# Optimization experiments

Measured on AMD Instinct MI355X. Metric: run time of the kernel, lower is better.

The kernel has to match this reference:

```python
import jax, jax.numpy as jnp
import numpy as np

E = 1024
H = 16
HD = E // H  # 64


def setup_inputs() -> dict:
    key = jax.random.key(0)
    ks = jax.random.split(key, 5)
    x = jax.random.normal(ks[0], (2, 2048, E), dtype=jnp.float32)
    s = 1.0 / np.sqrt(E)
    W_qkv = jax.random.uniform(ks[1], (E, 3 * E), jnp.float32, -s, s)
    b_qkv = jax.random.uniform(ks[2], (3 * E,), jnp.float32, -s, s)
    W_out = jax.random.uniform(ks[3], (E, E), jnp.float32, -s, s)
    b_out = jax.random.uniform(ks[4], (E,), jnp.float32, -s, s)
    return {"x": x, "W_qkv": W_qkv, "b_qkv": b_qkv, "W_out": W_out, "b_out": b_out}


def reference(x, W_qkv, b_qkv, W_out, b_out):
    B, N, _ = x.shape
    scale = HD ** (-0.5)
    qkv = x @ W_qkv + b_qkv                         # [B, N, 3E]
    qkv = qkv.reshape(B, N, H, 3 * HD)              # torch layout: per-head 3*hd chunk
    qkv = qkv.transpose(0, 2, 1, 3)                 # [B, H, N, 3*hd]
    q, k, v = jnp.split(qkv, 3, axis=-1)            # each [B, H, N, hd]
    attn = jnp.einsum('bhqd,bhkd->bhqk', q, k) * scale
    attn = jax.nn.softmax(attn, axis=-1)            # dropout is identity in eval
    out = jnp.einsum('bhqk,bhkd->bhqd', attn, v)    # [B, H, N, hd]
    out = out.transpose(0, 2, 1, 3).reshape(B, N, E)
    return out @ W_out + b_out
```

## Files before the change

kernel.cpp:

```cpp
#include <hip/hip_runtime.h>


#define SEQ 2048
#define NH  16

typedef __attribute__((ext_vector_type(8))) short short8;
typedef __attribute__((ext_vector_type(4))) short short4v;
typedef __attribute__((ext_vector_type(4))) float floatx4;
typedef __attribute__((ext_vector_type(4))) _Float16 half4;
typedef __attribute__((ext_vector_type(2))) _Float16 half2v;
typedef __attribute__((ext_vector_type(2))) __fp16 fp16x2;

#define QSCALE 0.1803368801111204f

__device__ __forceinline__ short f2bf(float f) {
    union { float f; unsigned u; } v; v.f = f;
    unsigned r = v.u + 0x7fffu + ((v.u >> 16) & 1u);
    return (short)(r >> 16);
}

__device__ __forceinline__ float fast_exp2(float x) {
#if __has_builtin(__builtin_amdgcn_exp2f)
    return __builtin_amdgcn_exp2f(x);
#else
    return exp2f(x);
#endif
}

__device__ __forceinline__ half2v cvt_pk(float a, float b) {
#if __has_builtin(__builtin_amdgcn_cvt_pkrtz)
    union { fp16x2 i; half2v o; } u;
    u.i = __builtin_amdgcn_cvt_pkrtz(a, b);
    return u.o;
#else
    half2v r; r.x = (_Float16)a; r.y = (_Float16)b; return r;
#endif
}

#define GLDS16(gp, lp)                                                          \
    __builtin_amdgcn_global_load_lds(                                           \
        (const __attribute__((address_space(1))) unsigned int*)(gp),            \
        (__attribute__((address_space(3))) unsigned int*)(lp), 16, 0, 0)

__global__ __launch_bounds__(256) void cast_f32_bf16_kernel(
    const float* __restrict__ in, short* __restrict__ out)
{
    int i = blockIdx.x * 256 + threadIdx.x;
    const float4* in4 = (const float4*)in + (size_t)i * 2;
    float4 a = in4[0], b = in4[1];
    short8 o = { f2bf(a.x), f2bf(a.y), f2bf(a.z), f2bf(a.w),
                 f2bf(b.x), f2bf(b.y), f2bf(b.z), f2bf(b.w) };
    *((short8*)out + i) = o;
}

__global__ __launch_bounds__(256) void transpose_cast_kernel(
    const float* __restrict__ in, short* __restrict__ out, int R, int C)
{
    __shared__ float T[64][65];
    const int tid = threadIdx.x;
    const int c0 = blockIdx.x * 64, r0 = blockIdx.y * 64;
#pragma unroll
    for (int it = 0; it < 4; ++it) {
        int r = it * 16 + (tid >> 4), c = (tid & 15) * 4;
        float4 v = *(const float4*)(in + (size_t)(r0 + r) * C + c0 + c);
        T[c+0][r] = v.x; T[c+1][r] = v.y; T[c+2][r] = v.z; T[c+3][r] = v.w;
    }
    __syncthreads();
#pragma unroll
    for (int it = 0; it < 4; ++it) {
        int oc = it * 16 + (tid >> 4), k = (tid & 15) * 4;
        short4v o = { f2bf(T[oc][k]), f2bf(T[oc][k+1]), f2bf(T[oc][k+2]), f2bf(T[oc][k+3]) };
        *(short4v*)(out + (size_t)(c0 + oc) * R + r0 + k) = o;
    }
}

__global__ __launch_bounds__(256) void vtrans_kernel(
    const _Float16* __restrict__ vn, _Float16* __restrict__ vt)
{
    __shared__ _Float16 T[64][72];
    const int tid = threadIdx.x;
    const int bh = blockIdx.y, n0 = blockIdx.x * 64;
#pragma unroll
    for (int it = 0; it < 2; ++it) {
        int n = it * 32 + (tid >> 3), c = (tid & 7) * 8;
        const _Float16* p = vn + ((size_t)bh * SEQ + n0 + n) * 64 + c;
        half4 a = *(const half4*)(p);
        half4 b = *(const half4*)(p + 4);
        T[c+0][n] = a.x; T[c+1][n] = a.y; T[c+2][n] = a.z; T[c+3][n] = a.w;
        T[c+4][n] = b.x; T[c+5][n] = b.y; T[c+6][n] = b.z; T[c+7][n] = b.w;
    }
    __syncthreads();
#pragma unroll
    for (int it = 0; it < 2; ++it) {
        int idx = it * 256 + tid;
        int quad = idx & 3, d = (idx >> 2) & 63, u = idx >> 8;
        const _Float16* row = &T[d][u * 32 + quad * 4];
        half4 lo = *(const half4*)(row);
        half4 hi = *(const half4*)(row + 16);
        _Float16* q = vt + ((size_t)bh * 64 + d) * SEQ + n0 + u * 32 + quad * 8;
        *(half4*)(q)     = lo;
        *(half4*)(q + 4) = hi;
    }
}

#define GEMM_CORE(A_PTR, B_PTR, LDA, LDB)                                        \
    __shared__ short As[128 * 32];                                               \
    __shared__ short Bs[128 * 32];                                               \
    const int tid  = threadIdx.x;                                                \
    const int lane = tid & 63, w = tid >> 6;                                     \
    const int quad = lane >> 4, l16 = lane & 15;                                 \
    const int wm = w >> 1, wn = w & 1;                                           \
    const int c0 = blockIdx.x * 128, r0 = blockIdx.y * 128;                      \
    floatx4 acc[4][4];                                                           \
    _Pragma("unroll")                                                            \
    for (int i = 0; i < 4; ++i)                                                  \
        _Pragma("unroll")                                                        \
        for (int j = 0; j < 4; ++j) acc[i][j] = (floatx4){0.f, 0.f, 0.f, 0.f};   \
    const int srow = tid >> 2;                                                   \
    const int sgx  = ((tid & 3) ^ ((srow >> 1) & 3)) * 8;                        \
    const short* Ag = (A_PTR) + (size_t)(r0 + srow) * (LDA) + sgx;               \
    const short* Bg = (B_PTR) + (size_t)(c0 + srow) * (LDB) + sgx;               \
    const int fsw = (l16 >> 1) & 3;                                              \
    for (int kk = 0; kk < 1024; kk += 32) {                                      \
        __syncthreads();                                                         \
        GLDS16(Ag + kk,                      As + tid * 8);                      \
        GLDS16(Ag + (size_t)64 * (LDA) + kk, As + 2048 + tid * 8);               \
        GLDS16(Bg + kk,                      Bs + tid * 8);                      \
        GLDS16(Bg + (size_t)64 * (LDB) + kk, Bs + 2048 + tid * 8);               \
        __syncthreads();                                                         \
        short8 af[4], bf[4];                                                     \
        _Pragma("unroll")                                                        \
        for (int mt = 0; mt < 4; ++mt)                                           \
            af[mt] = *(const short8*)&As[(wm * 64 + mt * 16 + l16) * 32 + (quad ^ fsw) * 8]; \
        _Pragma("unroll")                                                        \
        for (int nt = 0; nt < 4; ++nt)                                           \
            bf[nt] = *(const short8*)&Bs[(wn * 64 + nt * 16 + l16) * 32 + (quad ^ fsw) * 8]; \
        _Pragma("unroll")                                                        \
        for (int mt = 0; mt < 4; ++mt)                                           \
            _Pragma("unroll")                                                    \
            for (int nt = 0; nt < 4; ++nt)                                       \
                acc[mt][nt] = __builtin_amdgcn_mfma_f32_16x16x32_bf16(           \
                    af[mt], bf[nt], acc[mt][nt], 0, 0, 0);                       \
    }

__global__ __launch_bounds__(256) void qkv_gemm_kernel(
    const short* __restrict__ wt, const short* __restrict__ xb,
    const float* __restrict__ bias,
    short* __restrict__ qb, short* __restrict__ kb, _Float16* __restrict__ vnb)
{
    GEMM_CORE(wt, xb, 1024, 1024)
#pragma unroll
    for (int mt = 0; mt < 4; ++mt) {
        int oc0 = r0 + wm * 64 + mt * 16 + quad * 4;
        int head = oc0 / 192;
        int t = (oc0 - head * 192) >> 6;
        int d0 = oc0 & 63;
        float4 bv = *(const float4*)(bias + oc0);
#pragma unroll
        for (int nt = 0; nt < 4; ++nt) {
            int tok = c0 + wn * 64 + nt * 16 + l16;
            int bh = (tok >> 11) * NH + head;
            size_t base = ((size_t)bh * SEQ + (tok & (SEQ - 1))) * 64 + d0;
            float v0 = acc[mt][nt][0] + bv.x, v1 = acc[mt][nt][1] + bv.y;
            float v2 = acc[mt][nt][2] + bv.z, v3 = acc[mt][nt][3] + bv.w;
            if (t == 0) {
                short4v o = { f2bf(v0 * QSCALE), f2bf(v1 * QSCALE),
                              f2bf(v2 * QSCALE), f2bf(v3 * QSCALE) };
                *(short4v*)(qb + base) = o;
            } else if (t == 1) {
                short4v o = { f2bf(v0), f2bf(v1), f2bf(v2), f2bf(v3) };
                *(short4v*)(kb + base) = o;
            } else {
                half4 o = { (_Float16)v0, (_Float16)v1, (_Float16)v2, (_Float16)v3 };
                *(half4*)(vnb + base) = o;
            }
        }
    }
}

__global__ __launch_bounds__(512) void out_gemm_kernel(
    const short* __restrict__ wt, const short* __restrict__ ab,
    const float* __restrict__ bias, float* __restrict__ out)
{
    __shared__ short As[128 * 32];
    __shared__ short Bs[128 * 32];
    const int tid  = threadIdx.x;
    const int lane = tid & 63, w = tid >> 6;
    const int quad = lane >> 4, l16 = lane & 15;
    const int wm = w >> 2, wn = w & 3;
    const int c0 = blockIdx.x * 128, r0 = blockIdx.y * 128;
    floatx4 acc[4][2];
#pragma unroll
    for (int i = 0; i < 4; ++i)
#pragma unroll
        for (int j = 0; j < 2; ++j) acc[i][j] = (floatx4){0.f, 0.f, 0.f, 0.f};
    const int srow = tid >> 2;
    const int sgx  = ((tid & 3) ^ ((srow >> 1) & 3)) * 8;
    const short* Ag = wt + (size_t)(r0 + srow) * 1024 + sgx;
    const short* Bg = ab + (size_t)(c0 + srow) * 1024 + sgx;
    const int fsw = (l16 >> 1) & 3;
    for (int kk = 0; kk < 1024; kk += 32) {
        __syncthreads();
        GLDS16(Ag + kk, As + tid * 8);
        GLDS16(Bg + kk, Bs + tid * 8);
        __syncthreads();
        short8 af[4], bf[2];
#pragma unroll
        for (int mt = 0; mt < 4; ++mt)
            af[mt] = *(const short8*)&As[(wm * 64 + mt * 16 + l16) * 32 + (quad ^ fsw) * 8];
#pragma unroll
        for (int nt = 0; nt < 2; ++nt)
            bf[nt] = *(const short8*)&Bs[(wn * 32 + nt * 16 + l16) * 32 + (quad ^ fsw) * 8];
#pragma unroll
        for (int mt = 0; mt < 4; ++mt)
#pragma unroll
            for (int nt = 0; nt < 2; ++nt)
                acc[mt][nt] = __builtin_amdgcn_mfma_f32_16x16x32_bf16(
                    af[mt], bf[nt], acc[mt][nt], 0, 0, 0);
    }
#pragma unroll
    for (int mt = 0; mt < 4; ++mt) {
        int oc0 = r0 + wm * 64 + mt * 16 + quad * 4;
        float4 bv = *(const float4*)(bias + oc0);
#pragma unroll
        for (int nt = 0; nt < 2; ++nt) {
            int tok = c0 + wn * 32 + nt * 16 + l16;
            float4 o = { acc[mt][nt][0] + bv.x, acc[mt][nt][1] + bv.y,
                         acc[mt][nt][2] + bv.z, acc[mt][nt][3] + bv.w };
            *(float4*)(out + (size_t)tok * 1024 + oc0) = o;
        }
    }
}

__global__ __launch_bounds__(512) void attn_kernel(
    const short* __restrict__ qb, const short* __restrict__ kb,
    const _Float16* __restrict__ vtb, short* __restrict__ ob)
{
    __shared__ short    Ks[128 * 64];
    __shared__ _Float16 Vts[64 * 128];
    __shared__ float    Ls[8][32];
    const int tid  = threadIdx.x;
    const int lane = tid & 63, w = tid >> 6;
    const int quad = lane >> 4, l16 = lane & 15;
    const int qh = w >> 2, kq = w & 3;
    const int bh = blockIdx.x;
    const int q0 = blockIdx.y * 64;

    short8 aq[2][2];
#pragma unroll
    for (int qf = 0; qf < 2; ++qf) {
        const short* qp = qb + ((size_t)bh * SEQ + q0 + qh * 32 + qf * 16 + l16) * 64 + quad * 8;
        aq[qf][0] = *(const short8*)(qp);
        aq[qf][1] = *(const short8*)(qp + 32);
    }

    const int krow = tid >> 3, kg = tid & 7;
    const short* kgp = kb + ((size_t)bh * SEQ + krow) * 64 + (kg ^ (krow & 7)) * 8;
    const int vd = (tid >> 2) & 63, vgg = tid & 3, vu = tid >> 8;
    const _Float16* vgp = vtb + ((size_t)bh * 64 + vd) * SEQ + vu * 32
                        + (vgg ^ ((vd >> 1) & 3)) * 8;

    floatx4 o_acc[4][2];
#pragma unroll
    for (int dt = 0; dt < 4; ++dt)
#pragma unroll
        for (int qf = 0; qf < 2; ++qf) o_acc[dt][qf] = (floatx4){0.f, 0.f, 0.f, 0.f};
    float lw[2] = {0.f, 0.f};

    for (int k0 = 0; k0 < SEQ; k0 += 128) {
        __syncthreads();
        const short* kc_p = kgp + (size_t)k0 * 64;
        GLDS16(kc_p,        Ks + tid * 8);
        GLDS16(kc_p + 4096, Ks + 4096 + tid * 8);
        const _Float16* vc_p = vgp + k0;
        GLDS16((const short*)(vc_p),      (short*)Vts + tid * 8);
        GLDS16((const short*)(vc_p + 64), (short*)Vts + 4096 + tid * 8);
        __syncthreads();

        half4 avlo[4], avhi[4];
#pragma unroll
        for (int dt = 0; dt < 4; ++dt) {
            union { short8 s; struct { half4 lo; half4 hi; } h; } u;
            u.s = *(const short8*)((const short*)Vts + kq * 2048
                    + (dt * 16 + l16) * 32 + (quad ^ ((l16 >> 1) & 3)) * 8);
            avlo[dt] = u.h.lo; avhi[dt] = u.h.hi;
        }

#pragma unroll
        for (int kt = 0; kt < 2; ++kt) {
            const short* krp = &Ks[(kq * 32 + kt * 16 + l16) * 64];
            short8 ak0 = *(const short8*)(krp + ((0 + quad) ^ (l16 & 7)) * 8);
            short8 ak1 = *(const short8*)(krp + ((4 + quad) ^ (l16 & 7)) * 8);
            floatx4 sacc[2];
#pragma unroll
            for (int qf = 0; qf < 2; ++qf) {
                floatx4 z = (floatx4){0.f, 0.f, 0.f, 0.f};
                z = __builtin_amdgcn_mfma_f32_16x16x32_bf16(ak0, aq[qf][0], z, 0, 0, 0);
                sacc[qf] = __builtin_amdgcn_mfma_f32_16x16x32_bf16(ak1, aq[qf][1], z, 0, 0, 0);
            }
            half4 pf[2];
#pragma unroll
            for (int qf = 0; qf < 2; ++qf) {
                float p0 = fast_exp2(sacc[qf][0]);
                float p1 = fast_exp2(sacc[qf][1]);
                float p2 = fast_exp2(sacc[qf][2]);
                float p3 = fast_exp2(sacc[qf][3]);
                lw[qf] += (p0 + p1) + (p2 + p3);
                half2v lo = cvt_pk(p0, p1), hi = cvt_pk(p2, p3);
                pf[qf] = (half4){lo.x, lo.y, hi.x, hi.y};
            }
#pragma unroll
            for (int dt = 0; dt < 4; ++dt)
#pragma unroll
                for (int qf = 0; qf < 2; ++qf)
                    o_acc[dt][qf] = __builtin_amdgcn_mfma_f32_16x16x16f16(
                        kt ? avhi[dt] : avlo[dt], pf[qf], o_acc[dt][qf], 0, 0, 0);
        }
    }

#pragma unroll
    for (int qf = 0; qf < 2; ++qf) {
        lw[qf] += __shfl_xor(lw[qf], 16);
        lw[qf] += __shfl_xor(lw[qf], 32);
        if (quad == 0) Ls[w][qf * 16 + l16] = lw[qf];
    }

    float* RedA = (float*)Ks;
    float* RedB = (float*)Vts;
    __syncthreads();
#pragma unroll
    for (int dt = 0; dt < 4; ++dt)
#pragma unroll
        for (int qf = 0; qf < 2; ++qf) {
            int fi = (((qh * 2 + qf) * 4 + dt) * 64 + lane) * 4;
            if (kq == 2) *(floatx4*)&RedA[fi] = o_acc[dt][qf];
            if (kq == 3) *(floatx4*)&RedB[fi] = o_acc[dt][qf];
        }
    __syncthreads();
    if (kq == 0 || kq == 1) {
#pragma unroll
        for (int dt = 0; dt < 4; ++dt)
#pragma unroll
            for (int qf = 0; qf < 2; ++qf) {
                int fi = (((qh * 2 + qf) * 4 + dt) * 64 + lane) * 4;
                o_acc[dt][qf] += *(const floatx4*)((kq == 0) ? &RedA[fi] : &RedB[fi]);
                if (kq == 1) *(floatx4*)&RedB[fi] = o_acc[dt][qf];
            }
    }
    __syncthreads();
    if (kq == 0) {
        float inv[2];
#pragma unroll
        for (int qf = 0; qf < 2; ++qf) {
            int qi = qf * 16 + l16;
            inv[qf] = 1.0f / (Ls[qh * 4 + 0][qi] + Ls[qh * 4 + 1][qi]
                            + Ls[qh * 4 + 2][qi] + Ls[qh * 4 + 3][qi]);
        }
        const int b = bh >> 4, h = bh & 15;
#pragma unroll
        for (int dt = 0; dt < 4; ++dt)
#pragma unroll
            for (int qf = 0; qf < 2; ++qf) {
                int fi = (((qh * 2 + qf) * 4 + dt) * 64 + lane) * 4;
                floatx4 o = o_acc[dt][qf] + *(const floatx4*)&RedB[fi];
                int tok = b * SEQ + q0 + qh * 32 + qf * 16 + l16;
                short4v o4 = { f2bf(o[0] * inv[qf]), f2bf(o[1] * inv[qf]),
                               f2bf(o[2] * inv[qf]), f2bf(o[3] * inv[qf]) };
                *(short4v*)(ob + (size_t)tok * 1024 + h * 64 + dt * 16 + quad * 4) = o4;
            }
    }
}

extern "C" void kernel_launch(void* const* d_in, const int* in_sizes, int n_in,
                              void* d_out, int out_size, void* d_ws, size_t ws_size,
                              hipStream_t stream) {
    const float* x     = (const float*)d_in[0];
    const float* W_qkv = (const float*)d_in[1];
    const float* b_qkv = (const float*)d_in[2];
    const float* W_out = (const float*)d_in[3];
    const float* b_out = (const float*)d_in[4];
    float* out = (float*)d_out;

    short* xb      = (short*)d_ws;
    short* wqkvt   = xb    + (size_t)4096 * 1024;
    short* woutt   = wqkvt + (size_t)3072 * 1024;
    short* qb      = woutt + (size_t)1024 * 1024;
    short* kb      = qb    + (size_t)32 * SEQ * 64;
    _Float16* vnb  = (_Float16*)(kb + (size_t)32 * SEQ * 64);
    _Float16* vtb  = vnb + (size_t)32 * SEQ * 64;
    short* ob      = (short*)(vtb + (size_t)32 * 64 * SEQ);

    cast_f32_bf16_kernel<<<2048, 256, 0, stream>>>(x, xb);
    transpose_cast_kernel<<<dim3(48, 16), 256, 0, stream>>>(W_qkv, wqkvt, 1024, 3072);
    transpose_cast_kernel<<<dim3(16, 16), 256, 0, stream>>>(W_out, woutt, 1024, 1024);
    qkv_gemm_kernel<<<dim3(32, 24), 256, 0, stream>>>(wqkvt, xb, b_qkv, qb, kb, vnb);
    vtrans_kernel<<<dim3(32, 32), 256, 0, stream>>>(vnb, vtb);
    attn_kernel<<<dim3(32, 32), 512, 0, stream>>>(qb, kb, vtb, ob);
    out_gemm_kernel<<<dim3(32, 8), 512, 0, stream>>>(woutt, ob, b_out, out);
}
```

Measured before the change: 207.0 us.

## Fuse prep kernels and halve attention block size with two KV splits

Merges the x cast and the two weight transpose-casts into one launch dispatched by block index, removing two kernel launches. The attention kernel drops from 512 to 256 threads (4 waves), so each wave handles two 32-key chunks instead of one. The cross-wave reduction shrinks to a single exchange, and a min-blocks hint of 4 is added for occupancy. The grid axes are swapped so q-tiles of the same head are adjacent, which may help K/V cache reuse. Each thread now issues twice as many LDS copies per tile, and the reduction tail is shorter.

```diff
diff --git a/kernel.cpp b/kernel.cpp
--- a/kernel.cpp
+++ b/kernel.cpp
@@ -42,23 +42,31 @@
         (const __attribute__((address_space(1))) unsigned int*)(gp),            \
         (__attribute__((address_space(3))) unsigned int*)(lp), 16, 0, 0)
 
-__global__ __launch_bounds__(256) void cast_f32_bf16_kernel(
-    const float* __restrict__ in, short* __restrict__ out)
-{
-    int i = blockIdx.x * 256 + threadIdx.x;
-    const float4* in4 = (const float4*)in + (size_t)i * 2;
-    float4 a = in4[0], b = in4[1];
-    short8 o = { f2bf(a.x), f2bf(a.y), f2bf(a.z), f2bf(a.w),
-                 f2bf(b.x), f2bf(b.y), f2bf(b.z), f2bf(b.w) };
-    *((short8*)out + i) = o;
-}
-
-__global__ __launch_bounds__(256) void transpose_cast_kernel(
-    const float* __restrict__ in, short* __restrict__ out, int R, int C)
-{
+__global__ __launch_bounds__(256) void prep_kernel(
+    const float* __restrict__ x,  short* __restrict__ xb,
+    const float* __restrict__ wq, short* __restrict__ wqkvt,
+    const float* __restrict__ wo, short* __restrict__ woutt)
+{
+    const int tid = threadIdx.x;
+    const int b = blockIdx.x;
+    if (b < 2048) {
+        int i = b * 256 + tid;
+        const float4* in4 = (const float4*)x + (size_t)i * 2;
+        float4 a = in4[0], c = in4[1];
+        short8 o = { f2bf(a.x), f2bf(a.y), f2bf(a.z), f2bf(a.w),
+                     f2bf(c.x), f2bf(c.y), f2bf(c.z), f2bf(c.w) };
+        *((short8*)xb + i) = o;
+        return;
+    }
     __shared__ float T[64][65];
-    const int tid = threadIdx.x;
-    const int c0 = blockIdx.x * 64, r0 = blockIdx.y * 64;
+    const float* in; short* out; int R, C, c0, r0;
+    if (b < 2816) {
+        int t = b - 2048; in = wq; out = wqkvt; R = 1024; C = 3072;
+        c0 = (t % 48) * 64; r0 = (t / 48) * 64;
+    } else {
+        int t = b - 2816; in = wo; out = woutt; R = 1024; C = 1024;
+        c0 = (t & 15) * 64; r0 = (t >> 4) * 64;
+    }
 #pragma unroll
     for (int it = 0; it < 4; ++it) {
         int r = it * 16 + (tid >> 4), c = (tid & 15) * 4;
@@ -232,19 +240,19 @@
     }
 }
 
-__global__ __launch_bounds__(512) void attn_kernel(
+__global__ __launch_bounds__(256, 4) void attn_kernel(
     const short* __restrict__ qb, const short* __restrict__ kb,
     const _Float16* __restrict__ vtb, short* __restrict__ ob)
 {
     __shared__ short    Ks[128 * 64];
     __shared__ _Float16 Vts[64 * 128];
-    __shared__ float    Ls[8][32];
+    __shared__ float    Ls[4][32];
     const int tid  = threadIdx.x;
     const int lane = tid & 63, w = tid >> 6;
     const int quad = lane >> 4, l16 = lane & 15;
-    const int qh = w >> 2, kq = w & 3;
-    const int bh = blockIdx.x;
-    const int q0 = blockIdx.y * 64;
+    const int qh = w >> 1, kq = w & 1;
+    const int bh = blockIdx.y;
+    const int q0 = blockIdx.x * 64;
 
     short8 aq[2][2];
 #pragma unroll
@@ -256,9 +264,8 @@
 
     const int krow = tid >> 3, kg = tid & 7;
     const short* kgp = kb + ((size_t)bh * SEQ + krow) * 64 + (kg ^ (krow & 7)) * 8;
-    const int vd = (tid >> 2) & 63, vgg = tid & 3, vu = tid >> 8;
-    const _Float16* vgp = vtb + ((size_t)bh * 64 + vd) * SEQ + vu * 32
-                        + (vgg ^ ((vd >> 1) & 3)) * 8;
+    const int vd = tid >> 2, vgg = tid & 3;
+    const _Float16* vgp = vtb + ((size_t)bh * 64 + vd) * SEQ + (vgg ^ ((vd >> 1) & 3)) * 8;
 
     floatx4 o_acc[4][2];
 #pragma unroll
@@ -271,50 +278,57 @@
         __syncthreads();
         const short* kc_p = kgp + (size_t)k0 * 64;
         GLDS16(kc_p,        Ks + tid * 8);
+        GLDS16(kc_p + 2048, Ks + 2048 + tid * 8);
         GLDS16(kc_p + 4096, Ks + 4096 + tid * 8);
+        GLDS16(kc_p + 6144, Ks + 6144 + tid * 8);
         const _Float16* vc_p = vgp + k0;
         GLDS16((const short*)(vc_p),      (short*)Vts + tid * 8);
+        GLDS16((const short*)(vc_p + 32), (short*)Vts + 2048 + tid * 8);
         GLDS16((const short*)(vc_p + 64), (short*)Vts + 4096 + tid * 8);
+        GLDS16((const short*)(vc_p + 96), (short*)Vts + 6144 + tid * 8);
         __syncthreads();
 
-        half4 avlo[4], avhi[4];
-#pragma unroll
-        for (int dt = 0; dt < 4; ++dt) {
-            union { short8 s; struct { half4 lo; half4 hi; } h; } u;
-            u.s = *(const short8*)((const short*)Vts + kq * 2048
-                    + (dt * 16 + l16) * 32 + (quad ^ ((l16 >> 1) & 3)) * 8);
-            avlo[dt] = u.h.lo; avhi[dt] = u.h.hi;
-        }
-
-#pragma unroll
-        for (int kt = 0; kt < 2; ++kt) {
-            const short* krp = &Ks[(kq * 32 + kt * 16 + l16) * 64];
-            short8 ak0 = *(const short8*)(krp + ((0 + quad) ^ (l16 & 7)) * 8);
-            short8 ak1 = *(const short8*)(krp + ((4 + quad) ^ (l16 & 7)) * 8);
-            floatx4 sacc[2];
-#pragma unroll
-            for (int qf = 0; qf < 2; ++qf) {
-                floatx4 z = (floatx4){0.f, 0.f, 0.f, 0.f};
-                z = __builtin_amdgcn_mfma_f32_16x16x32_bf16(ak0, aq[qf][0], z, 0, 0, 0);
-                sacc[qf] = __builtin_amdgcn_mfma_f32_16x16x32_bf16(ak1, aq[qf][1], z, 0, 0, 0);
+#pragma unroll
+        for (int uu = 0; uu < 2; ++uu) {
+            const int u = kq * 2 + uu;
+            half4 avlo[4], avhi[4];
+#pragma unroll
+            for (int dt = 0; dt < 4; ++dt) {
+                union { short8 s; struct { half4 lo; half4 hi; } h; } vv;
+                vv.s = *(const short8*)((const short*)Vts + u * 2048
+                        + (dt * 16 + l16) * 32 + (quad ^ ((l16 >> 1) & 3)) * 8);
+                avlo[dt] = vv.h.lo; avhi[dt] = vv.h.hi;
             }
-            half4 pf[2];
-#pragma unroll
-            for (int qf = 0; qf < 2; ++qf) {
-                float p0 = fast_exp2(sacc[qf][0]);
-                float p1 = fast_exp2(sacc[qf][1]);
-                float p2 = fast_exp2(sacc[qf][2]);
-                float p3 = fast_exp2(sacc[qf][3]);
-                lw[qf] += (p0 + p1) + (p2 + p3);
-                half2v lo = cvt_pk(p0, p1), hi = cvt_pk(p2, p3);
-                pf[qf] = (half4){lo.x, lo.y, hi.x, hi.y};
+#pragma unroll
+            for (int h = 0; h < 2; ++h) {
+                const short* krp = &Ks[(u * 32 + h * 16 + l16) * 64];
+                short8 ak0 = *(const short8*)(krp + ((0 + quad) ^ (l16 & 7)) * 8);
+                short8 ak1 = *(const short8*)(krp + ((4 + quad) ^ (l16 & 7)) * 8);
+                floatx4 sacc[2];
+#pragma unroll
+                for (int qf = 0; qf < 2; ++qf) {
+                    floatx4 z = (floatx4){0.f, 0.f, 0.f, 0.f};
+                    z = __builtin_amdgcn_mfma_f32_16x16x32_bf16(ak0, aq[qf][0], z, 0, 0, 0);
+                    sacc[qf] = __builtin_amdgcn_mfma_f32_16x16x32_bf16(ak1, aq[qf][1], z, 0, 0, 0);
+                }
+                half4 pf[2];
+#pragma unroll
+                for (int qf = 0; qf < 2; ++qf) {
+                    float p0 = fast_exp2(sacc[qf][0]);
+                    float p1 = fast_exp2(sacc[qf][1]);
+                    float p2 = fast_exp2(sacc[qf][2]);
+                    float p3 = fast_exp2(sacc[qf][3]);
+                    lw[qf] += (p0 + p1) + (p2 + p3);
+                    half2v lo = cvt_pk(p0, p1), hi = cvt_pk(p2, p3);
+                    pf[qf] = (half4){lo.x, lo.y, hi.x, hi.y};
+                }
+#pragma unroll
+                for (int dt = 0; dt < 4; ++dt)
+#pragma unroll
+                    for (int qf = 0; qf < 2; ++qf)
+                        o_acc[dt][qf] = __builtin_amdgcn_mfma_f32_16x16x16f16(
+                            h ? avhi[dt] : avlo[dt], pf[qf], o_acc[dt][qf], 0, 0, 0);
             }
-#pragma unroll
-            for (int dt = 0; dt < 4; ++dt)
-#pragma unroll
-                for (int qf = 0; qf < 2; ++qf)
-                    o_acc[dt][qf] = __builtin_amdgcn_mfma_f32_16x16x16f16(
-                        kt ? avhi[dt] : avlo[dt], pf[qf], o_acc[dt][qf], 0, 0, 0);
         }
     }
 
@@ -325,36 +339,22 @@
         if (quad == 0) Ls[w][qf * 16 + l16] = lw[qf];
     }
 
-    float* RedA = (float*)Ks;
-    float* RedB = (float*)Vts;
+    float* Red = (float*)Ks;
     __syncthreads();
 #pragma unroll
     for (int dt = 0; dt < 4; ++dt)
 #pragma unroll
         for (int qf = 0; qf < 2; ++qf) {
             int fi = (((qh * 2 + qf) * 4 + dt) * 64 + lane) * 4;
-            if (kq == 2) *(floatx4*)&RedA[fi] = o_acc[dt][qf];
-            if (kq == 3) *(floatx4*)&RedB[fi] = o_acc[dt][qf];
-        }
-    __syncthreads();
-    if (kq == 0 || kq == 1) {
-#pragma unroll
-        for (int dt = 0; dt < 4; ++dt)
-#pragma unroll
-            for (int qf = 0; qf < 2; ++qf) {
-                int fi = (((qh * 2 + qf) * 4 + dt) * 64 + lane) * 4;
-                o_acc[dt][qf] += *(const floatx4*)((kq == 0) ? &RedA[fi] : &RedB[fi]);
-                if (kq == 1) *(floatx4*)&RedB[fi] = o_acc[dt][qf];
-            }
-    }
+            if (kq == 1) *(floatx4*)&Red[fi] = o_acc[dt][qf];
+        }
     __syncthreads();
     if (kq == 0) {
         float inv[2];
 #pragma unroll
         for (int qf = 0; qf < 2; ++qf) {
             int qi = qf * 16 + l16;
-            inv[qf] = 1.0f / (Ls[qh * 4 + 0][qi] + Ls[qh * 4 + 1][qi]
-                            + Ls[qh * 4 + 2][qi] + Ls[qh * 4 + 3][qi]);
+            inv[qf] = 1.0f / (Ls[qh * 2 + 0][qi] + Ls[qh * 2 + 1][qi]);
         }
         const int b = bh >> 4, h = bh & 15;
 #pragma unroll
@@ -362,7 +362,7 @@
 #pragma unroll
             for (int qf = 0; qf < 2; ++qf) {
                 int fi = (((qh * 2 + qf) * 4 + dt) * 64 + lane) * 4;
-                floatx4 o = o_acc[dt][qf] + *(const floatx4*)&RedB[fi];
+                floatx4 o = o_acc[dt][qf] + *(const floatx4*)&Red[fi];
                 int tok = b * SEQ + q0 + qh * 32 + qf * 16 + l16;
                 short4v o4 = { f2bf(o[0] * inv[qf]), f2bf(o[1] * inv[qf]),
                                f2bf(o[2] * inv[qf]), f2bf(o[3] * inv[qf]) };
@@ -390,11 +390,9 @@
     _Float16* vtb  = vnb + (size_t)32 * SEQ * 64;
     short* ob      = (short*)(vtb + (size_t)32 * 64 * SEQ);
 
-    cast_f32_bf16_kernel<<<2048, 256, 0, stream>>>(x, xb);
-    transpose_cast_kernel<<<dim3(48, 16), 256, 0, stream>>>(W_qkv, wqkvt, 1024, 3072);
-    transpose_cast_kernel<<<dim3(16, 16), 256, 0, stream>>>(W_out, woutt, 1024, 1024);
+    prep_kernel<<<3072, 256, 0, stream>>>(x, xb, W_qkv, wqkvt, W_out, woutt);
     qkv_gemm_kernel<<<dim3(32, 24), 256, 0, stream>>>(wqkvt, xb, b_qkv, qb, kb, vnb);
     vtrans_kernel<<<dim3(32, 32), 256, 0, stream>>>(vnb, vtb);
-    attn_kernel<<<dim3(32, 32), 512, 0, stream>>>(qb, kb, vtb, ob);
+    attn_kernel<<<dim3(32, 32), 256, 0, stream>>>(qb, kb, vtb, ob);
     out_gemm_kernel<<<dim3(32, 8), 512, 0, stream>>>(woutt, ob, b_out, out);
 }
```

Measured after the change: 196.6 us. 5.0% less time.
